# Kernel optimization log

Measured on AMD Instinct MI355X. Metric: run time of the kernel, lower is better.

The kernel has to match this reference:

```python
import jax, jax.numpy as jnp
import numpy as np

NUM_CLASSES = 100  # static stand-in for int(max(label)+1)


def setup_inputs() -> dict:
    key = jax.random.key(0)
    k1, k2 = jax.random.split(key)
    feat = jax.random.normal(k1, (500000, 256), dtype=jnp.float32)
    label = jax.random.randint(k2, (500000,), 0, NUM_CLASSES, dtype=jnp.int64)
    return {"feat": feat, "label": label}


def reference(feat, label):
    # Per-class centers via segment mean (replaces the per-class python loop)
    counts = jax.ops.segment_sum(jnp.ones((feat.shape[0],), feat.dtype), label,
                                 num_segments=NUM_CLASSES)  # [C]
    centers = jax.ops.segment_sum(feat, label, num_segments=NUM_CLASSES)
    centers = centers / counts[:, None]  # [C, D]

    # ||f - c||_2 for all (sample, class) pairs without a [N, C, D] intermediate:
    # ||f||^2 - 2 f.c + ||c||^2
    sq_f = jnp.sum(feat * feat, axis=1, keepdims=True)          # [N, 1]
    sq_c = jnp.sum(centers * centers, axis=1)                    # [C]
    d2 = sq_f - 2.0 * (feat @ centers.T) + sq_c[None, :]         # [N, C]
    dist = jnp.sqrt(jnp.maximum(d2, 0.0))

    # distance of each sample to its own class center (margin=False branch)
    given = jnp.take_along_axis(dist, label[:, None], axis=1)[:, 0]  # [N]
    return given
```

## Files before the change

kernel.cpp:

```cpp
#include <hip/hip_runtime.h>
#include <math.h>

#define REALC  100
#define NCLASS 104
#define DIM    256
#define CPLANE (NCLASS * 64)
#define TBL    (2 * CPLANE)

#define BLOCK  256
#define B1     1024
#define G1CH   128

#define SCALE    256.0f
#define INVSCALE (1.0f / 256.0f)

#define WS_COUNTS  0
#define WS_FLAG    NCLASS
#define WS_CENTERS 128
#define WS_PART    (128 + NCLASS * DIM)

__global__ __launch_bounds__(BLOCK) void k0_init(int* __restrict__ counts,
                                                 int* __restrict__ flag,
                                                 const unsigned int* __restrict__ lab,
                                                 int n) {
    int t = threadIdx.x;
    if (t < NCLASS) counts[t] = 0;
    __shared__ unsigned int any_nonzero;
    if (t == 0) any_nonzero = 0u;
    __syncthreads();
    unsigned int v = 0u;
    int limit = min(1024, (n - 1) / 2);
    for (int i = t; i < limit; i += BLOCK) v |= lab[2 * i + 1];
    if (v) atomicOr(&any_nonzero, 1u);
    __syncthreads();
    if (t == 0) *flag = (any_nonzero == 0u) ? 1 : 0;
}

__global__ __launch_bounds__(B1, 4) void k1_accum(const float* __restrict__ feat,
                                                  const unsigned int* __restrict__ lab,
                                                  const int* __restrict__ flag,
                                                  int* __restrict__ part,
                                                  int* __restrict__ counts,
                                                  int n) {
    __shared__ __align__(16) int lsum[TBL];
    __shared__ int lcnt[NCLASS];
    int t = threadIdx.x, lane = t & 63, w = t >> 6;
    int chunk = blockIdx.x >> 1, half = blockIdx.x & 1;
    int is64 = *flag;

    for (int i = t; i < TBL; i += B1) lsum[i] = 0;
    if (t < NCLASS) lcnt[t] = 0;
    __syncthreads();

    int rpb = (n + G1CH - 1) / G1CH;
    int r0 = chunk * rpb, r1 = min(n, r0 + rpb);

    const float2* f2 = (const float2*)feat;
    int colbase = (half << 6) + lane;

    for (int bstart = r0 + (w << 6); bstart < r1; bstart += B1) {
        int jmax = min(64, r1 - bstart);
        int lv = 0;
        if (lane < jmax) {
            int idx = bstart + lane;
            int v = is64 ? (int)lab[2 * (size_t)idx] : (int)lab[idx];
            lv = min(max(v, 0), NCLASS - 1);
            if (half == 0) atomicAdd(&lcnt[lv], 1);
        }
        const float2* rp = f2 + (size_t)bstart * 128 + colbase;
        if (jmax == 64) {
#pragma unroll 16
            for (int j = 0; j < 64; j++) {
                int cls = __shfl(lv, j);
                float2 a = rp[(size_t)j * 128];
                int ix = __float2int_rn(a.x * SCALE);
                int iy = __float2int_rn(a.y * SCALE);
                atomicAdd(&lsum[(cls << 6) + lane], ix);
                atomicAdd(&lsum[CPLANE + (cls << 6) + lane], iy);
            }
        } else {
            for (int j = 0; j < jmax; j++) {
                int cls = __shfl(lv, j);
                float2 a = rp[(size_t)j * 128];
                int ix = __float2int_rn(a.x * SCALE);
                int iy = __float2int_rn(a.y * SCALE);
                atomicAdd(&lsum[(cls << 6) + lane], ix);
                atomicAdd(&lsum[CPLANE + (cls << 6) + lane], iy);
            }
        }
    }
    __syncthreads();

    int4* pb = (int4*)(part + (size_t)blockIdx.x * TBL);
    const int4* ls = (const int4*)lsum;
    for (int i = t; i < TBL / 4; i += B1) pb[i] = ls[i];

    if (half == 0 && t < NCLASS) {
        int v = lcnt[t];
        if (v) atomicAdd(&counts[t], v);
    }
}

__global__ __launch_bounds__(BLOCK) void k2_reduce(const int* __restrict__ part,
                                                   const int* __restrict__ counts,
                                                   float* __restrict__ centers) {
    int i = blockIdx.x * BLOCK + threadIdx.x;
    if (i >= NCLASS * DIM) return;
    int h = (i >= TBL) ? 1 : 0;
    int j = i - h * TBL;
    const int* p0 = part + (size_t)h * TBL + j;
    int acc = 0;
#pragma unroll 8
    for (int k = 0; k < G1CH; k++) acc += p0[(size_t)(2 * k) * TBL];

    int p = (j >= CPLANE) ? 1 : 0;
    int r = j - p * CPLANE;
    int c = r >> 6, l = r & 63;
    int col = (h << 7) + (l << 1) + p;
    float cnt = (float)counts[c];
    centers[c * DIM + col] = ((float)acc * INVSCALE) / fmaxf(cnt, 1.0f);
}

__global__ __launch_bounds__(BLOCK, 4) void k3_dist(const float* __restrict__ feat,
                                                    const unsigned int* __restrict__ lab,
                                                    const int* __restrict__ flag,
                                                    const float* __restrict__ centers,
                                                    float* __restrict__ out,
                                                    int n) {
    __shared__ float dbuf[4][64];
    int t = threadIdx.x, lane = t & 63, w = t >> 6;
    int base = (blockIdx.x * 4 + w) * 64;
    if (base >= n) return;
    int is64 = *flag;

    int idx = base + lane;
    int lv = 0;
    if (idx < n) {
        int v = is64 ? (int)lab[2 * (size_t)idx] : (int)lab[idx];
        lv = min(max(v, 0), NCLASS - 1);
    }

    const float4* f4 = (const float4*)feat;
    const float4* c4 = (const float4*)centers;
    int rend = min(64, n - base);

    if (rend == 64) {
        int g = lane >> 4, s = lane & 15;
#pragma unroll 2
        for (int i = 0; i < 16; i++) {
            int r = 4 * i + g;
            int cls = __shfl(lv, r);
            const float4* fr = f4 + (size_t)(base + r) * 64 + s;
            const float4* cr = c4 + (size_t)cls * 64 + s;
            float p = 0.0f;
#pragma unroll
            for (int k = 0; k < 4; k++) {
                float4 a = fr[16 * k];
                float4 c = cr[16 * k];
                float dx = a.x - c.x, dy = a.y - c.y, dz = a.z - c.z, dw = a.w - c.w;
                p = fmaf(dx, dx, p); p = fmaf(dy, dy, p);
                p = fmaf(dz, dz, p); p = fmaf(dw, dw, p);
            }
            p += __shfl_xor(p, 1);
            p += __shfl_xor(p, 2);
            p += __shfl_xor(p, 4);
            p += __shfl_xor(p, 8);
            if (s == 0) dbuf[w][r] = p;
        }
        out[base + lane] = sqrtf(dbuf[w][lane]);
    } else {
        for (int j = 0; j < rend; j++) {
            int cls = __shfl(lv, j);
            float4 a = f4[(size_t)(base + j) * 64 + lane];
            float4 c = c4[(size_t)cls * 64 + lane];
            float dx = a.x - c.x, dy = a.y - c.y, dz = a.z - c.z, dw = a.w - c.w;
            float p = fmaf(dx, dx, fmaf(dy, dy, fmaf(dz, dz, dw * dw)));
#pragma unroll
            for (int off = 32; off > 0; off >>= 1) p += __shfl_down(p, off);
            if (lane == 0) dbuf[w][j] = p;
        }
        if (lane < rend) out[base + lane] = sqrtf(dbuf[w][lane]);
    }
}

extern "C" void kernel_launch(void* const* d_in, const int* in_sizes, int n_in,
                              void* d_out, int out_size, void* d_ws, size_t ws_size,
                              hipStream_t stream) {
    const float* feat = (const float*)d_in[0];
    const unsigned int* lab = (const unsigned int*)d_in[1];
    int n = in_sizes[0] / DIM;

    int* ws = (int*)d_ws;
    int* counts = ws + WS_COUNTS;
    int* flag = ws + WS_FLAG;
    float* centers = (float*)(ws + WS_CENTERS);
    int* part = ws + WS_PART;
    float* out = (float*)d_out;

    k0_init<<<1, BLOCK, 0, stream>>>(counts, flag, lab, n);

    k1_accum<<<G1CH * 2, B1, 0, stream>>>(feat, lab, flag, part, counts, n);

    k2_reduce<<<(NCLASS * DIM + BLOCK - 1) / BLOCK, BLOCK, 0, stream>>>(part, counts, centers);

    int ntiles = (n + 63) >> 6;
    k3_dist<<<(ntiles + 3) >> 2, BLOCK, 0, stream>>>(feat, lab, flag, centers, out, n);
}
```

Before: 789.8 us.

## Stage centers in LDS for distance kernel and double accumulation grid

The distance kernel now copies the full centers table (about 104 KB) into shared memory once per 1024-thread block and reads class centers from LDS instead of global memory. Each wave handles one 64-row tile with a full-row float4 layout, reducing each row with butterfly shuffles into a per-lane register, which removes the dbuf shared buffer. The accumulation kernel grid is doubled (G1CH 256) with a higher occupancy hint. The risk is that the large LDS footprint limits blocks per CU and the table load is repeated for every block, while the extra partial tables make the reduction kernel do more work.

```diff
diff --git a/kernel.cpp b/kernel.cpp
--- a/kernel.cpp
+++ b/kernel.cpp
@@ -9,7 +9,8 @@
 
 #define BLOCK  256
 #define B1     1024
-#define G1CH   128
+#define G1CH   256
+#define B3     1024
 
 #define SCALE    256.0f
 #define INVSCALE (1.0f / 256.0f)
@@ -36,7 +37,7 @@
     if (t == 0) *flag = (any_nonzero == 0u) ? 1 : 0;
 }
 
-__global__ __launch_bounds__(B1, 4) void k1_accum(const float* __restrict__ feat,
+__global__ __launch_bounds__(B1, 8) void k1_accum(const float* __restrict__ feat,
                                                   const unsigned int* __restrict__ lab,
                                                   const int* __restrict__ flag,
                                                   int* __restrict__ part,
@@ -121,65 +122,74 @@
     centers[c * DIM + col] = ((float)acc * INVSCALE) / fmaxf(cnt, 1.0f);
 }
 
-__global__ __launch_bounds__(BLOCK, 4) void k3_dist(const float* __restrict__ feat,
-                                                    const unsigned int* __restrict__ lab,
-                                                    const int* __restrict__ flag,
-                                                    const float* __restrict__ centers,
-                                                    float* __restrict__ out,
-                                                    int n) {
-    __shared__ float dbuf[4][64];
+__global__ __launch_bounds__(B3, 4) void k3_dist(const float* __restrict__ feat,
+                                                 const unsigned int* __restrict__ lab,
+                                                 const int* __restrict__ flag,
+                                                 const float* __restrict__ centers,
+                                                 float* __restrict__ out,
+                                                 int n) {
+    __shared__ __align__(16) float ldsC[NCLASS * DIM];
     int t = threadIdx.x, lane = t & 63, w = t >> 6;
-    int base = (blockIdx.x * 4 + w) * 64;
+
+    {
+        const float4* cg = (const float4*)centers;
+        float4* cl = (float4*)ldsC;
+        for (int i = t; i < NCLASS * DIM / 4; i += B3) cl[i] = cg[i];
+    }
+    __syncthreads();
+
+    int tile = blockIdx.x * 16 + w;
+    int base = tile << 6;
     if (base >= n) return;
     int is64 = *flag;
-
-    int idx = base + lane;
+    int rend = min(64, n - base);
+
     int lv = 0;
-    if (idx < n) {
+    if (lane < rend) {
+        int idx = base + lane;
         int v = is64 ? (int)lab[2 * (size_t)idx] : (int)lab[idx];
         lv = min(max(v, 0), NCLASS - 1);
     }
 
     const float4* f4 = (const float4*)feat;
-    const float4* c4 = (const float4*)centers;
-    int rend = min(64, n - base);
+    const float4* lc4 = (const float4*)ldsC;
+    float dmine = 0.0f;
 
     if (rend == 64) {
-        int g = lane >> 4, s = lane & 15;
 #pragma unroll 2
-        for (int i = 0; i < 16; i++) {
-            int r = 4 * i + g;
-            int cls = __shfl(lv, r);
-            const float4* fr = f4 + (size_t)(base + r) * 64 + s;
-            const float4* cr = c4 + (size_t)cls * 64 + s;
-            float p = 0.0f;
+        for (int j0 = 0; j0 < 64; j0 += 4) {
+            float p[4];
 #pragma unroll
-            for (int k = 0; k < 4; k++) {
-                float4 a = fr[16 * k];
-                float4 c = cr[16 * k];
+            for (int u = 0; u < 4; u++) {
+                int cls = __shfl(lv, j0 + u);
+                float4 a = f4[(size_t)(base + j0 + u) * 64 + lane];
+                float4 c = lc4[cls * 64 + lane];
                 float dx = a.x - c.x, dy = a.y - c.y, dz = a.z - c.z, dw = a.w - c.w;
-                p = fmaf(dx, dx, p); p = fmaf(dy, dy, p);
-                p = fmaf(dz, dz, p); p = fmaf(dw, dw, p);
-            }
-            p += __shfl_xor(p, 1);
-            p += __shfl_xor(p, 2);
-            p += __shfl_xor(p, 4);
-            p += __shfl_xor(p, 8);
-            if (s == 0) dbuf[w][r] = p;
-        }
-        out[base + lane] = sqrtf(dbuf[w][lane]);
+                p[u] = fmaf(dx, dx, fmaf(dy, dy, fmaf(dz, dz, dw * dw)));
+            }
+#pragma unroll
+            for (int u = 0; u < 4; u++) {
+                float q = p[u];
+                q += __shfl_xor(q, 1);  q += __shfl_xor(q, 2);
+                q += __shfl_xor(q, 4);  q += __shfl_xor(q, 8);
+                q += __shfl_xor(q, 16); q += __shfl_xor(q, 32);
+                if (lane == j0 + u) dmine = q;
+            }
+        }
+        out[base + lane] = sqrtf(dmine);
     } else {
         for (int j = 0; j < rend; j++) {
             int cls = __shfl(lv, j);
             float4 a = f4[(size_t)(base + j) * 64 + lane];
-            float4 c = c4[(size_t)cls * 64 + lane];
+            float4 c = lc4[cls * 64 + lane];
             float dx = a.x - c.x, dy = a.y - c.y, dz = a.z - c.z, dw = a.w - c.w;
-            float p = fmaf(dx, dx, fmaf(dy, dy, fmaf(dz, dz, dw * dw)));
-#pragma unroll
-            for (int off = 32; off > 0; off >>= 1) p += __shfl_down(p, off);
-            if (lane == 0) dbuf[w][j] = p;
-        }
-        if (lane < rend) out[base + lane] = sqrtf(dbuf[w][lane]);
+            float q = fmaf(dx, dx, fmaf(dy, dy, fmaf(dz, dz, dw * dw)));
+            q += __shfl_xor(q, 1);  q += __shfl_xor(q, 2);
+            q += __shfl_xor(q, 4);  q += __shfl_xor(q, 8);
+            q += __shfl_xor(q, 16); q += __shfl_xor(q, 32);
+            if (lane == j) dmine = q;
+        }
+        if (lane < rend) out[base + lane] = sqrtf(dmine);
     }
 }
 
@@ -204,5 +214,6 @@
     k2_reduce<<<(NCLASS * DIM + BLOCK - 1) / BLOCK, BLOCK, 0, stream>>>(part, counts, centers);
 
     int ntiles = (n + 63) >> 6;
-    k3_dist<<<(ntiles + 3) >> 2, BLOCK, 0, stream>>>(feat, lab, flag, centers, out, n);
-}
+    int nb3 = (ntiles + 15) >> 4;
+    k3_dist<<<nb3, B3, 0, stream>>>(feat, lab, flag, centers, out, n);
+}
```

After: 764.3 us. -3.2%, faster.
